# Kernel optimization log

Hardware: AMD Instinct MI355X
Metric: run time of the kernel (lower is better)

Reference implementation:

```python
import jax, jax.numpy as jnp
import numpy as np

TEMP = 0.1
EDGE_THR = 0.25
PATCH = 16
SAMPLE = 100
EPS = 1e-12


def _split_into_patches(feats, P):
    # replicates torch unfold(2).unfold(3).unfold(4).contiguous().view(B,-1,C,P,P,P)
    B, C, D, H, W = feats.shape
    x = feats.reshape(B, C, D // P, P, H // P, P, W // P, P)
    x = x.transpose(0, 1, 2, 4, 6, 3, 5, 7)  # [B,C,Dp,Hp,Wp,P,P,P]
    return x.reshape(B, -1, C, P, P, P)       # C-order reshape == torch .view on contiguous


def _projector(x, w1, b1, w2, b2):
    # torch Linear: y = x @ W.T + b
    h = jax.nn.relu(jnp.matmul(x, w1.T) + b1)
    return jnp.matmul(h, w2.T) + b2


def _normalize(x, axis):
    n = jnp.sqrt(jnp.sum(x * x, axis=axis, keepdims=True))
    return x / jnp.maximum(n, EPS)


def _conv3d(x, w, b, padding):
    y = jax.lax.conv_general_dilated(
        x, w, window_strides=(1, 1, 1), padding=padding,
        dimension_numbers=('NCDHW', 'OIDHW', 'NCDHW'))
    return y + b[None, :, None, None, None]


def setup_inputs() -> dict:
    key = jax.random.key(0)
    ks = jax.random.split(key, 12)
    B, C, D, H, W = 2, 128, 64, 64, 64
    inp = {
        'anchor_feats': jax.random.normal(ks[0], (B, C, D, H, W), dtype=jnp.float32),
        'positive_feats': jax.random.normal(ks[1], (B, C, D, H, W), dtype=jnp.float32),
        'conv1_w': jax.random.normal(ks[2], (32, C, 3, 3, 3), dtype=jnp.float32) * 0.02,
        'conv1_b': jnp.zeros((32,), dtype=jnp.float32),
        'conv2_w': jax.random.normal(ks[3], (1, 32, 1, 1, 1), dtype=jnp.float32) * 0.1,
        'conv2_b': jnp.zeros((1,), dtype=jnp.float32),
        'proj_w1': jax.random.normal(ks[4], (C, C), dtype=jnp.float32) * (1.0 / np.sqrt(C)),
        'proj_b1': jnp.zeros((C,), dtype=jnp.float32),
        'proj_w2': jax.random.normal(ks[5], (64, C), dtype=jnp.float32) * (1.0 / np.sqrt(C)),
        'proj_b2': jnp.zeros((64,), dtype=jnp.float32),
        'loss_weights': jnp.array([1.0, 0.7], dtype=jnp.float32),
        'voxel_idx': jax.random.permutation(ks[6], PATCH ** 3)[:SAMPLE].astype(jnp.int64),
    }
    return inp


def reference(anchor_feats, positive_feats, conv1_w, conv1_b, conv2_w, conv2_b,
              proj_w1, proj_b1, proj_w2, proj_b2, loss_weights, voxel_idx):
    B, C, D, H, W = anchor_feats.shape
    P = PATCH

    # region classifier: Conv3d(C,32,3,p=1) -> ReLU -> Conv3d(32,1,1) -> Sigmoid
    h = jax.nn.relu(_conv3d(anchor_feats, conv1_w, conv1_b, ((1, 1), (1, 1), (1, 1))))
    region_probs = jax.nn.sigmoid(_conv3d(h, conv2_w, conv2_b, ((0, 0), (0, 0), (0, 0))))
    region_mask = (region_probs > EDGE_THR).astype(jnp.float32)  # [B,1,D,H,W]

    anchor_p = _split_into_patches(anchor_feats, P)    # [B,N,C,P,P,P]
    positive_p = _split_into_patches(positive_feats, P)
    region_p = _split_into_patches(region_mask, P)     # [B,N,1,P,P,P]

    edge_ratio = jnp.mean(region_p, axis=(2, 3, 4, 5))  # [B,N]
    mask_vox = (edge_ratio > 0.6).astype(jnp.float32)
    mask_patch = (edge_ratio < 0.4).astype(jnp.float32)

    # ---- patch-level contrast (vectorized over B,N) ----
    a_vec = jnp.mean(anchor_p, axis=(3, 4, 5))    # [B,N,C]
    p_vec = jnp.mean(positive_p, axis=(3, 4, 5))
    a_proj = _normalize(_projector(a_vec, proj_w1, proj_b1, proj_w2, proj_b2), -1)
    p_proj = _normalize(_projector(p_vec, proj_w1, proj_b1, proj_w2, proj_b2), -1)
    patch_losses = -jnp.sum(a_proj * p_proj, axis=-1) / TEMP  # [B,N]

    # ---- voxel-level contrast (vectorized over B,N) ----
    N = anchor_p.shape[1]
    a_vox = anchor_p.reshape(B, N, C, P ** 3).transpose(0, 1, 3, 2)[:, :, voxel_idx, :]  # [B,N,S,C]
    p_vox = positive_p.reshape(B, N, C, P ** 3).transpose(0, 1, 3, 2)[:, :, voxel_idx, :]
    a_vp = _normalize(_projector(a_vox, proj_w1, proj_b1, proj_w2, proj_b2), -1)  # [B,N,S,64]
    p_vp = _normalize(_projector(p_vox, proj_w1, proj_b1, proj_w2, proj_b2), -1)
    sim = jnp.einsum('bnsd,bntd->bnst', a_vp, p_vp) / TEMP  # [B,N,S,S]
    lse = jax.nn.logsumexp(sim, axis=-1)                    # [B,N,S]
    diag = jnp.diagonal(sim, axis1=-2, axis2=-1)            # [B,N,S]
    vox_losses = jnp.mean(lse - diag, axis=-1)              # [B,N]

    patch_sum = jnp.sum(patch_losses * mask_patch)
    vox_sum = jnp.sum(vox_losses * mask_vox)
    valid = jnp.sum(mask_patch) + jnp.sum(mask_vox)

    total = (loss_weights[0] * patch_sum + loss_weights[1] * vox_sum)
    return jnp.where(valid > 0, total / jnp.maximum(valid, 1.0), 0.0)
```

## Files before the change

kernel.cpp:

```cpp
#include <hip/hip_runtime.h>

using short8 = __attribute__((ext_vector_type(8))) short;
using f32x16 = __attribute__((ext_vector_type(16))) float;

#define THR_LOGIT (-1.0986122886681098f)
#define ZPAGE_OFF 156509184

__device__ __forceinline__ unsigned short f2bf(float f) {
  unsigned u = __float_as_uint(f);
  u = (u + 0x7FFFu + ((u >> 16) & 1u)) >> 16;
  return (unsigned short)u;
}

__device__ __forceinline__ void async_copy16(void* lds, const void* g) {
  __builtin_amdgcn_global_load_lds(
      (const __attribute__((address_space(1))) unsigned int*)g,
      (__attribute__((address_space(3))) unsigned int*)lds, 16, 0, 0);
}

__global__ void __launch_bounds__(256) k_prep(const float* __restrict__ c1w,
    const float* __restrict__ pw1, const float* __restrict__ pw2,
    short* __restrict__ wt2, float* __restrict__ w1t, float* __restrict__ w2t) {
  int i = blockIdx.x * 256 + threadIdx.x;
  if (i < 110592) {
    int j8 = i & 7, l31v = (i >> 3) & 31, halfv = (i >> 8) & 1;
    int q = i >> 9;
    int dz = q % 3; q /= 3;
    int dx = q % 3; q /= 3;
    int dy = q % 3; int co8 = q / 3;
    int c = co8 * 16 + halfv * 8 + j8;
    int tap = dz * 9 + dy * 3 + dx;
    wt2[i] = (short)f2bf(c1w[l31v * 3456 + c * 27 + tap]);
  } else if (i < 126976) {
    int i2 = i - 110592; int c = i2 >> 7; int j = i2 & 127;
    w1t[i2] = pw1[j * 128 + c];
  } else if (i < 135168) {
    int i3 = i - 126976; int j = i3 >> 6; int d = i3 & 63;
    w2t[i3] = pw2[d * 128 + j];
  }
}

__global__ void k_inv(const int* __restrict__ vidx, int* __restrict__ inv) {
  int t = threadIdx.x;
  for (int k = t; k < 4096; k += 256) inv[k] = -1;
  __syncthreads();
  if (t < 100) inv[vidx[t]] = t;
}

__global__ void __launch_bounds__(256) k_stage(const float* __restrict__ src,
    short* __restrict__ in2, float* __restrict__ S4, float* __restrict__ Xmat,
    const int* __restrict__ inv, int vox_row_base) {
  __shared__ float tile[128][65];
  __shared__ int mcnt;
  __shared__ int mx[64];
  __shared__ int mrow[64];
  int bi = blockIdx.x;
  int b = bi >> 8, z = (bi >> 2) & 63, yp = bi & 3;
  int t = threadIdx.x;
  int zp = z >> 4, pz = z & 15;
  int cc = t & 127, xh = t >> 7;
  float part0 = 0.f, part1 = 0.f;

  for (int y0 = 0; y0 < 16; ++y0) {
    int y = yp * 16 + y0;
    __syncthreads();
    if (t == 0) mcnt = 0;
    {
      int x = t & 63, w = t >> 6;
      const float* sp = src + (long)b * 128 * 262144 + (long)z * 4096 + (long)y * 64 + x;
      #pragma unroll 4
      for (int it = 0; it < 32; ++it) {
        int c = it * 4 + w;
        tile[c][x] = sp[(long)c * 262144];
      }
    }
    __syncthreads();
    if (in2 != nullptr) {
      long rowbase = ((long)(b * 64 + z) * 64 + y) * 8192;
      int x = t >> 2, q = t & 3;
      int slot = (q & 1) ^ ((x >> 2) & 1);
      #pragma unroll
      for (int i = 0; i < 4; ++i) {
        int co8 = i * 2 + (q >> 1);
        short8 pk;
        #pragma unroll
        for (int j = 0; j < 8; ++j) pk[j] = (short)f2bf(tile[i * 32 + q * 8 + j][x]);
        *(short8*)(in2 + rowbase + co8 * 1024 + x * 16 + slot * 8) = pk;
      }
    }
    {
      float s0 = 0.f, s1 = 0.f;
      #pragma unroll
      for (int px = 0; px < 16; ++px) s0 += tile[cc][(xh * 2) * 16 + px];
      #pragma unroll
      for (int px = 0; px < 16; ++px) s1 += tile[cc][(xh * 2 + 1) * 16 + px];
      part0 += s0; part1 += s1;
    }
    if (t < 64) {
      int s = inv[pz * 256 + y0 * 16 + (t & 15)];
      if (s >= 0) {
        int idx = atomicAdd(&mcnt, 1);
        mx[idx] = t;
        int n = zp * 16 + yp * 4 + (t >> 4);
        mrow[idx] = vox_row_base + (b * 64 + n) * 100 + s;
      }
    }
    __syncthreads();
    int mc = mcnt;
    for (int i = 0; i < mc; ++i) {
      if (t < 128) Xmat[(long)mrow[i] * 128 + t] = tile[t][mx[i]];
    }
  }
  long sb = ((long)(b * 64 + z) * 4 + yp) * 512;
  S4[sb + cc * 4 + xh * 2 + 0] = part0;
  S4[sb + cc * 4 + xh * 2 + 1] = part1;
}

__global__ void __launch_bounds__(256, 3) k_conv(const short* __restrict__ in2,
    const short* __restrict__ wt2, const float* __restrict__ c1b,
    const float* __restrict__ c2w, const float* __restrict__ c2b,
    int* __restrict__ counts) {
  extern __shared__ char smem[];
  __shared__ int lcnt[4];
  int bi0 = blockIdx.x;
  int bi = ((bi0 & 7) << 8) | (bi0 >> 3);
  int b = bi >> 10, zb = (bi >> 5) & 31, yg = bi & 31;
  int z0 = zb * 2, y0 = yg * 2;
  int tid = threadIdx.x;
  int lane = tid & 63;
  int l31 = lane & 31, half = lane >> 5;
  int wave = tid >> 6;
  int xh = wave & 1, yo = wave >> 1;

  if (tid < 4) lcnt[tid] = 0;
  *(int*)(smem + 32768 + tid * 4) = 0;
  int zoff = 32768 + lane * 16;

  int gbase[8];
  int gmask[8];
  #pragma unroll
  for (int k = 0; k < 8; ++k) {
    int g = k * 256 + tid;
    int row = g >> 7, pos = g & 127;
    int zz = z0 - 1 + (row >> 2);
    int yy = y0 - 1 + (row & 3);
    bool v = ((unsigned)zz < 64u) && ((unsigned)yy < 64u);
    gbase[k] = v ? (((b * 64 + zz) * 64 + yy) * 16384 + pos * 16)
                 : (ZPAGE_OFF + pos * 16);
    gmask[k] = v ? -1 : 0;
  }
  const char* gsrc = (const char*)in2;

  int xbase = xh * 32 + l31;
  int offA[3];
  int vmA[3];
  #pragma unroll
  for (int d = 0; d < 3; ++d) {
    int xp = xbase + d - 1;
    bool v = (unsigned)xp < 64u;
    int xc = min(max(xp, 0), 63);
    offA[d] = v ? (xc * 32 + ((half ^ ((xc >> 2) & 1)) << 4)) : zoff;
    vmA[d] = v ? -1 : 0;
  }
  int yb = yo * 2048;

  f32x16 acc0 = {}, acc1 = {};

  #pragma unroll
  for (int k = 0; k < 8; ++k)
    async_copy16(smem + (k * 256 + tid) * 16, gsrc + gbase[k]);
  __syncthreads();

  for (int co8 = 0; co8 < 8; ++co8) {
    #pragma unroll
    for (int dy = 0; dy < 3; ++dy) {
      #pragma unroll
      for (int dx = 0; dx < 3; ++dx) {
        const short8* pB = (const short8*)wt2 +
            (((co8 * 9 + dy * 3 + dx) * 3) * 2 + half) * 32 + l31;
        short8 b0 = pB[0];
        short8 b1 = pB[64];
        short8 b2 = pB[128];
        int rb = dy * 2048 + yb;
        int m = vmA[dx], o = offA[dx];
        short8 a0 = *(const short8*)(smem + (((rb)          & m) + o));
        short8 a1 = *(const short8*)(smem + (((rb +  8192)  & m) + o));
        short8 a2 = *(const short8*)(smem + (((rb + 16384)  & m) + o));
        short8 a3 = *(const short8*)(smem + (((rb + 24576)  & m) + o));
        acc0 = __builtin_amdgcn_mfma_f32_32x32x16_bf16(a0, b0, acc0, 0, 0, 0);
        acc1 = __builtin_amdgcn_mfma_f32_32x32x16_bf16(a1, b0, acc1, 0, 0, 0);
        acc0 = __builtin_amdgcn_mfma_f32_32x32x16_bf16(a1, b1, acc0, 0, 0, 0);
        acc1 = __builtin_amdgcn_mfma_f32_32x32x16_bf16(a2, b1, acc1, 0, 0, 0);
        acc0 = __builtin_amdgcn_mfma_f32_32x32x16_bf16(a2, b2, acc0, 0, 0, 0);
        acc1 = __builtin_amdgcn_mfma_f32_32x32x16_bf16(a3, b2, acc1, 0, 0, 0);
      }
    }
    __syncthreads();
    if (co8 < 7) {
      int cadd = (co8 + 1) * 2048;
      #pragma unroll
      for (int k = 0; k < 8; ++k)
        async_copy16(smem + (k * 256 + tid) * 16,
                     gsrc + gbase[k] + (cadd & gmask[k]));
      __syncthreads();
    }
  }

  float b1v = c1b[l31];
  float w2v = c2w[l31];
  float b2v = c2b[0];
  int cnt0 = 0, cnt1 = 0;
  #pragma unroll
  for (int za = 0; za < 2; ++za) {
    #pragma unroll
    for (int r = 0; r < 16; ++r) {
      float v = fmaxf((za ? acc1[r] : acc0[r]) + b1v, 0.f) * w2v;
      v += __shfl_xor(v, 1);
      v += __shfl_xor(v, 2);
      v += __shfl_xor(v, 4);
      v += __shfl_xor(v, 8);
      v += __shfl_xor(v, 16);
      int bit = (v + b2v) > THR_LOGIT;
      if (r < 8) cnt0 += bit; else cnt1 += bit;
    }
  }
  if (l31 == 0) {
    atomicAdd(&lcnt[xh * 2 + 0], cnt0);
    atomicAdd(&lcnt[xh * 2 + 1], cnt1);
  }
  __syncthreads();
  if (tid < 4) {
    int n = (zb >> 3) * 16 + (yg >> 3) * 4 + tid;
    atomicAdd(&counts[b * 64 + n], lcnt[tid]);
  }
}

__global__ void __launch_bounds__(256) k_vecreduce(const float* __restrict__ S4a,
    const float* __restrict__ S4p, float* __restrict__ Xmat) {
  int g = blockIdx.x * 256 + threadIdx.x;
  int ten = g >> 14, rem = g & 16383;
  int b = rem >> 13, n = (rem >> 7) & 63, c = rem & 127;
  int zp = n >> 4, yp = (n >> 2) & 3, xp = n & 3;
  const float* S = ten ? S4p : S4a;
  float s = 0.f;
  #pragma unroll
  for (int k = 0; k < 16; ++k)
    s += S[((long)(b * 64 + zp * 16 + k) * 4 + yp) * 512 + c * 4 + xp];
  Xmat[(long)(ten * 128 + b * 64 + n) * 128 + c] = s * (1.f / 4096.f);
}

__global__ void __launch_bounds__(256) k_proj(const float* __restrict__ Xmat,
    const float* __restrict__ w1t, const float* __restrict__ pb1,
    const float* __restrict__ w2t, const float* __restrict__ pb2,
    float* __restrict__ P) {
  __shared__ float xsT[128][20];
  __shared__ float hsT[128][20];
  __shared__ float os[16][68];
  int bi = blockIdx.x;
  long row0 = (long)bi * 16;
  int t = threadIdx.x;
  {
    int r = t >> 4, c0 = (t & 15) * 8;
    const float* xp = Xmat + (row0 + r) * 128 + c0;
    #pragma unroll
    for (int k = 0; k < 8; ++k) xsT[c0 + k][r] = xp[k];
  }
  __syncthreads();
  {
    int j = t & 127, rh = t >> 7;
    float hacc[8];
    float bb = pb1[j];
    #pragma unroll
    for (int r8 = 0; r8 < 8; ++r8) hacc[r8] = bb;
    for (int c = 0; c < 128; ++c) {
      float w = w1t[c * 128 + j];
      float4 xlo = *(const float4*)&xsT[c][rh * 8];
      float4 xhi = *(const float4*)&xsT[c][rh * 8 + 4];
      hacc[0] += xlo.x * w; hacc[1] += xlo.y * w; hacc[2] += xlo.z * w; hacc[3] += xlo.w * w;
      hacc[4] += xhi.x * w; hacc[5] += xhi.y * w; hacc[6] += xhi.z * w; hacc[7] += xhi.w * w;
    }
    #pragma unroll
    for (int r8 = 0; r8 < 8; ++r8) hsT[j][rh * 8 + r8] = fmaxf(hacc[r8], 0.f);
  }
  __syncthreads();
  {
    int d = t & 63, rq = t >> 6;
    float oacc[4];
    float bb = pb2[d];
    #pragma unroll
    for (int r4 = 0; r4 < 4; ++r4) oacc[r4] = bb;
    for (int j = 0; j < 128; ++j) {
      float w = w2t[j * 64 + d];
      float4 hv = *(const float4*)&hsT[j][rq * 4];
      oacc[0] += hv.x * w; oacc[1] += hv.y * w; oacc[2] += hv.z * w; oacc[3] += hv.w * w;
    }
    #pragma unroll
    for (int r4 = 0; r4 < 4; ++r4) os[rq * 4 + r4][d] = oacc[r4];
  }
  __syncthreads();
  {
    int r = t >> 4, dg = t & 15;
    float4 v = *(const float4*)&os[r][dg * 4];
    float ss = v.x * v.x + v.y * v.y + v.z * v.z + v.w * v.w;
    ss += __shfl_xor(ss, 1); ss += __shfl_xor(ss, 2);
    ss += __shfl_xor(ss, 4); ss += __shfl_xor(ss, 8);
    float sc = 1.f / fmaxf(sqrtf(ss), 1e-12f);
    float4 o; o.x = v.x * sc; o.y = v.y * sc; o.z = v.z * sc; o.w = v.w * sc;
    *(float4*)&P[(row0 + r) * 64 + dg * 4] = o;
  }
}

__global__ void __launch_bounds__(128) k_sim(const float* __restrict__ P,
                                             float* __restrict__ vloss) {
  __shared__ float ps[100][68];
  __shared__ float red[128];
  int bn = blockIdx.x;
  int t = threadIdx.x;
  long pbase = (long)(13056 + bn * 100) * 64;
  for (int i = t; i < 1600; i += 128) {
    int r = i >> 4, dg = i & 15;
    *(float4*)&ps[r][dg * 4] = *(const float4*)&P[pbase + r * 64 + dg * 4];
  }
  float4 areg[16];
  long abase = (long)(256 + bn * 100) * 64;
  if (t < 100) {
    #pragma unroll
    for (int j = 0; j < 16; ++j) areg[j] = *(const float4*)&P[abase + (long)t * 64 + j * 4];
  }
  __syncthreads();
  float res = 0.f;
  if (t < 100) {
    float m = -1e30f, sum = 0.f, diag = 0.f;
    for (int t2 = 0; t2 < 100; ++t2) {
      float d = 0.f;
      #pragma unroll
      for (int j = 0; j < 16; ++j) {
        float4 pv = *(const float4*)&ps[t2][j * 4];
        d += areg[j].x * pv.x + areg[j].y * pv.y + areg[j].z * pv.z + areg[j].w * pv.w;
      }
      float sim = d * 10.f;
      if (t2 == t) diag = sim;
      float nm = fmaxf(m, sim);
      sum = sum * __expf(m - nm) + __expf(sim - nm);
      m = nm;
    }
    res = m + logf(sum) - diag;
  }
  red[t] = res;
  __syncthreads();
  if (t == 0) {
    float s = 0.f;
    for (int i = 0; i < 100; ++i) s += red[i];
    vloss[bn] = s * 0.01f;
  }
}

__global__ void __launch_bounds__(128) k_final(const float* __restrict__ P,
    const float* __restrict__ vloss, const int* __restrict__ counts,
    const float* __restrict__ lw, float* __restrict__ out) {
  int t = threadIdx.x;
  int lane = t & 63;
  float pterm = 0.f, vterm = 0.f; int vcnt = 0;
  {
    int c = counts[t];
    bool maskv = c >= 2458;
    bool maskp = c <= 1638;
    float d = 0.f;
    for (int k = 0; k < 64; ++k) d += P[t * 64 + k] * P[(128 + t) * 64 + k];
    if (maskp) { pterm = -d * 10.f; vcnt += 1; }
    if (maskv) { vterm = vloss[t];  vcnt += 1; }
  }
  for (int m = 1; m < 64; m <<= 1) {
    pterm += __shfl_xor(pterm, m);
    vterm += __shfl_xor(vterm, m);
    vcnt  += __shfl_xor(vcnt, m);
  }
  __shared__ float sp[2], sv[2]; __shared__ int sc[2];
  if (lane == 0) { sp[t >> 6] = pterm; sv[t >> 6] = vterm; sc[t >> 6] = vcnt; }
  __syncthreads();
  if (t == 0) {
    float psum = sp[0] + sp[1], vsum = sv[0] + sv[1];
    int vc = sc[0] + sc[1];
    float total = lw[0] * psum + lw[1] * vsum;
    out[0] = (vc > 0) ? total / (float)vc : 0.f;
  }
}

extern "C" void kernel_launch(void* const* d_in, const int* in_sizes, int n_in,
                              void* d_out, int out_size, void* d_ws, size_t ws_size,
                              hipStream_t stream) {
  const float* anchor   = (const float*)d_in[0];
  const float* positive = (const float*)d_in[1];
  const float* c1w = (const float*)d_in[2];
  const float* c1b = (const float*)d_in[3];
  const float* c2w = (const float*)d_in[4];
  const float* c2b = (const float*)d_in[5];
  const float* pw1 = (const float*)d_in[6];
  const float* pb1 = (const float*)d_in[7];
  const float* pw2 = (const float*)d_in[8];
  const float* pb2 = (const float*)d_in[9];
  const float* lw  = (const float*)d_in[10];
  const int*   vidx = (const int*)d_in[11];

  char* ws = (char*)d_ws;
  short* in2   = (short*)(ws + 0);
  float* S4a   = (float*)(ws + 134217728);
  float* S4p   = (float*)(ws + 135266304);
  float* X     = (float*)(ws + 136314880);
  float* P     = (float*)(ws + 149553152);
  short* wt2   = (short*)(ws + 156172288);
  float* w1t   = (float*)(ws + 156393472);
  float* w2t   = (float*)(ws + 156459008);
  int*   inv   = (int*)  (ws + 156491776);
  int*   counts= (int*)  (ws + 156508160);
  float* vloss = (float*)(ws + 156508672);
  short* zpage = (short*)(ws + ZPAGE_OFF);

  hipFuncSetAttribute(reinterpret_cast<const void*>(k_conv),
                      hipFuncAttributeMaxDynamicSharedMemorySize, 33792);

  hipMemsetAsync(counts, 0, 128 * sizeof(int), stream);
  hipMemsetAsync(zpage, 0, 16384, stream);
  k_prep<<<528, 256, 0, stream>>>(c1w, pw1, pw2, wt2, w1t, w2t);
  k_inv<<<1, 256, 0, stream>>>(vidx, inv);
  k_stage<<<512, 256, 0, stream>>>(anchor,   in2,     S4a, X, inv, 256);
  k_stage<<<512, 256, 0, stream>>>(positive, nullptr, S4p, X, inv, 13056);
  k_conv<<<2048, 256, 33792, stream>>>(in2, wt2, c1b, c2w, c2b, counts);
  k_vecreduce<<<128, 256, 0, stream>>>(S4a, S4p, X);
  k_proj<<<1616, 256, 0, stream>>>(X, w1t, pb1, w2t, pb2, P);
  k_sim<<<128, 128, 0, stream>>>(P, vloss);
  k_final<<<1, 128, 0, stream>>>(P, vloss, counts, lw, (float*)d_out);
}
```

Baseline: 447.1 us.

## Enlarge conv3d block tile to 2x4 rows with register-cached A fragments

The conv kernel now gives each block a 2(z)x4(y) output tile instead of 2x2, staging a 4x6 halo slab in LDS, and each wave computes a 2x2 grid of 32x32 accumulators. A fragments for all dz/dy shifts are loaded into registers once per dx and reused across the 3x3 dz/dy taps, with one weight fragment feeding four MFMAs. This cuts the halo reload overhead and the LDS and weight load traffic per MFMA. In exchange it uses more LDS and registers (occupancy lowered to 2 blocks per SIMD target), launches half as many blocks, and adds s_setprio hints around the MFMA cluster.

```diff
diff --git a/kernel.cpp b/kernel.cpp
--- a/kernel.cpp
+++ b/kernel.cpp
@@ -116,16 +116,16 @@
   S4[sb + cc * 4 + xh * 2 + 1] = part1;
 }
 
-__global__ void __launch_bounds__(256, 3) k_conv(const short* __restrict__ in2,
+__global__ void __launch_bounds__(256, 2) k_conv(const short* __restrict__ in2,
     const short* __restrict__ wt2, const float* __restrict__ c1b,
     const float* __restrict__ c2w, const float* __restrict__ c2b,
     int* __restrict__ counts) {
   extern __shared__ char smem[];
   __shared__ int lcnt[4];
   int bi0 = blockIdx.x;
-  int bi = ((bi0 & 7) << 8) | (bi0 >> 3);
-  int b = bi >> 10, zb = (bi >> 5) & 31, yg = bi & 31;
-  int z0 = zb * 2, y0 = yg * 2;
+  int bi = ((bi0 & 7) << 7) | (bi0 >> 3);
+  int b = bi >> 9, zb = (bi >> 4) & 31, yg = bi & 15;
+  int z0 = zb * 2, y0 = yg * 4;
   int tid = threadIdx.x;
   int lane = tid & 63;
   int l31 = lane & 31, half = lane >> 5;
@@ -133,17 +133,17 @@
   int xh = wave & 1, yo = wave >> 1;
 
   if (tid < 4) lcnt[tid] = 0;
-  *(int*)(smem + 32768 + tid * 4) = 0;
-  int zoff = 32768 + lane * 16;
-
-  int gbase[8];
-  int gmask[8];
+  *(int*)(smem + 49152 + tid * 4) = 0;
+  int zoff = 49152 + lane * 16;
+
+  int gbase[12];
+  int gmask[12];
   #pragma unroll
-  for (int k = 0; k < 8; ++k) {
+  for (int k = 0; k < 12; ++k) {
     int g = k * 256 + tid;
     int row = g >> 7, pos = g & 127;
-    int zz = z0 - 1 + (row >> 2);
-    int yy = y0 - 1 + (row & 3);
+    int zz = z0 - 1 + row / 6;
+    int yy = y0 - 1 + row % 6;
     bool v = ((unsigned)zz < 64u) && ((unsigned)yy < 64u);
     gbase[k] = v ? (((b * 64 + zz) * 64 + yy) * 16384 + pos * 16)
                  : (ZPAGE_OFF + pos * 16);
@@ -162,44 +162,46 @@
     offA[d] = v ? (xc * 32 + ((half ^ ((xc >> 2) & 1)) << 4)) : zoff;
     vmA[d] = v ? -1 : 0;
   }
-  int yb = yo * 2048;
-
-  f32x16 acc0 = {}, acc1 = {};
+  int ybase = yo * 4096;
+  const short8* pBbase = (const short8*)wt2 + half * 32 + l31;
+
+  f32x16 acc[2][2] = {};
 
   #pragma unroll
-  for (int k = 0; k < 8; ++k)
+  for (int k = 0; k < 12; ++k)
     async_copy16(smem + (k * 256 + tid) * 16, gsrc + gbase[k]);
   __syncthreads();
 
   for (int co8 = 0; co8 < 8; ++co8) {
     #pragma unroll
-    for (int dy = 0; dy < 3; ++dy) {
-      #pragma unroll
-      for (int dx = 0; dx < 3; ++dx) {
-        const short8* pB = (const short8*)wt2 +
-            (((co8 * 9 + dy * 3 + dx) * 3) * 2 + half) * 32 + l31;
-        short8 b0 = pB[0];
-        short8 b1 = pB[64];
-        short8 b2 = pB[128];
-        int rb = dy * 2048 + yb;
-        int m = vmA[dx], o = offA[dx];
-        short8 a0 = *(const short8*)(smem + (((rb)          & m) + o));
-        short8 a1 = *(const short8*)(smem + (((rb +  8192)  & m) + o));
-        short8 a2 = *(const short8*)(smem + (((rb + 16384)  & m) + o));
-        short8 a3 = *(const short8*)(smem + (((rb + 24576)  & m) + o));
-        acc0 = __builtin_amdgcn_mfma_f32_32x32x16_bf16(a0, b0, acc0, 0, 0, 0);
-        acc1 = __builtin_amdgcn_mfma_f32_32x32x16_bf16(a1, b0, acc1, 0, 0, 0);
-        acc0 = __builtin_amdgcn_mfma_f32_32x32x16_bf16(a1, b1, acc0, 0, 0, 0);
-        acc1 = __builtin_amdgcn_mfma_f32_32x32x16_bf16(a2, b1, acc1, 0, 0, 0);
-        acc0 = __builtin_amdgcn_mfma_f32_32x32x16_bf16(a2, b2, acc0, 0, 0, 0);
-        acc1 = __builtin_amdgcn_mfma_f32_32x32x16_bf16(a3, b2, acc1, 0, 0, 0);
-      }
+    for (int dx = 0; dx < 3; ++dx) {
+      int m = vmA[dx], o = offA[dx];
+      short8 A[4][4];
+      #pragma unroll
+      for (int zs = 0; zs < 4; ++zs)
+        #pragma unroll
+        for (int yr = 0; yr < 4; ++yr)
+          A[zs][yr] = *(const short8*)(smem +
+              (((zs * 12288 + yr * 2048) + ybase) & m) + o);
+      __builtin_amdgcn_s_setprio(1);
+      #pragma unroll
+      for (int dz = 0; dz < 3; ++dz) {
+        #pragma unroll
+        for (int dy = 0; dy < 3; ++dy) {
+          short8 bf = pBbase[((co8 * 9 + dy * 3 + dx) * 3 + dz) * 64];
+          acc[0][0] = __builtin_amdgcn_mfma_f32_32x32x16_bf16(A[dz + 0][dy + 0], bf, acc[0][0], 0, 0, 0);
+          acc[1][0] = __builtin_amdgcn_mfma_f32_32x32x16_bf16(A[dz + 1][dy + 0], bf, acc[1][0], 0, 0, 0);
+          acc[0][1] = __builtin_amdgcn_mfma_f32_32x32x16_bf16(A[dz + 0][dy + 1], bf, acc[0][1], 0, 0, 0);
+          acc[1][1] = __builtin_amdgcn_mfma_f32_32x32x16_bf16(A[dz + 1][dy + 1], bf, acc[1][1], 0, 0, 0);
+        }
+      }
+      __builtin_amdgcn_s_setprio(0);
     }
     __syncthreads();
     if (co8 < 7) {
       int cadd = (co8 + 1) * 2048;
       #pragma unroll
-      for (int k = 0; k < 8; ++k)
+      for (int k = 0; k < 12; ++k)
         async_copy16(smem + (k * 256 + tid) * 16,
                      gsrc + gbase[k] + (cadd & gmask[k]));
       __syncthreads();
@@ -211,17 +213,20 @@
   float b2v = c2b[0];
   int cnt0 = 0, cnt1 = 0;
   #pragma unroll
-  for (int za = 0; za < 2; ++za) {
-    #pragma unroll
-    for (int r = 0; r < 16; ++r) {
-      float v = fmaxf((za ? acc1[r] : acc0[r]) + b1v, 0.f) * w2v;
-      v += __shfl_xor(v, 1);
-      v += __shfl_xor(v, 2);
-      v += __shfl_xor(v, 4);
-      v += __shfl_xor(v, 8);
-      v += __shfl_xor(v, 16);
-      int bit = (v + b2v) > THR_LOGIT;
-      if (r < 8) cnt0 += bit; else cnt1 += bit;
+  for (int zi = 0; zi < 2; ++zi) {
+    #pragma unroll
+    for (int yi = 0; yi < 2; ++yi) {
+      #pragma unroll
+      for (int r = 0; r < 16; ++r) {
+        float v = fmaxf(acc[zi][yi][r] + b1v, 0.f) * w2v;
+        v += __shfl_xor(v, 1);
+        v += __shfl_xor(v, 2);
+        v += __shfl_xor(v, 4);
+        v += __shfl_xor(v, 8);
+        v += __shfl_xor(v, 16);
+        int bit = (v + b2v) > THR_LOGIT;
+        if (r < 8) cnt0 += bit; else cnt1 += bit;
+      }
     }
   }
   if (l31 == 0) {
@@ -230,7 +235,7 @@
   }
   __syncthreads();
   if (tid < 4) {
-    int n = (zb >> 3) * 16 + (yg >> 3) * 4 + tid;
+    int n = (zb >> 3) * 16 + (yg >> 2) * 4 + tid;
     atomicAdd(&counts[b * 64 + n], lcnt[tid]);
   }
 }
@@ -417,7 +422,7 @@
   short* zpage = (short*)(ws + ZPAGE_OFF);
 
   hipFuncSetAttribute(reinterpret_cast<const void*>(k_conv),
-                      hipFuncAttributeMaxDynamicSharedMemorySize, 33792);
+                      hipFuncAttributeMaxDynamicSharedMemorySize, 50176);
 
   hipMemsetAsync(counts, 0, 128 * sizeof(int), stream);
   hipMemsetAsync(zpage, 0, 16384, stream);
@@ -425,7 +430,7 @@
   k_inv<<<1, 256, 0, stream>>>(vidx, inv);
   k_stage<<<512, 256, 0, stream>>>(anchor,   in2,     S4a, X, inv, 256);
   k_stage<<<512, 256, 0, stream>>>(positive, nullptr, S4p, X, inv, 13056);
-  k_conv<<<2048, 256, 33792, stream>>>(in2, wt2, c1b, c2w, c2b, counts);
+  k_conv<<<1024, 256, 50176, stream>>>(in2, wt2, c1b, c2w, c2b, counts);
   k_vecreduce<<<128, 256, 0, stream>>>(S4a, S4p, X);
   k_proj<<<1616, 256, 0, stream>>>(X, w1t, pb1, w2t, pb2, P);
   k_sim<<<128, 128, 0, stream>>>(P, vloss);
```

Result: faster. 424.8 us (-5.0%).
